# Performance work log

Measured on AMD Instinct MI355X. Metric: run time of the kernel, lower is better.

Reference implementation:

```python
import jax, jax.numpy as jnp
import numpy as np

BN_EPS = 1e-3  # keras BatchNormalization default epsilon


def setup_inputs() -> dict:
    key = jax.random.key(0)
    ks = jax.random.split(key, 7)
    B, W, D, H, C = 2, 32, 32, 32, 256
    x = jax.random.normal(ks[0], (B, W, D, H, C), dtype=jnp.float32)
    # Stacked params for the 4 branches: [query, key, judge, value]
    conv_w = jax.random.normal(ks[1], (4, C, C), dtype=jnp.float32) / np.sqrt(C).astype(np.float32)
    conv_b = jax.random.normal(ks[2], (4, C), dtype=jnp.float32) * 0.01
    bn_scale = 1.0 + 0.1 * jax.random.normal(ks[3], (4, C), dtype=jnp.float32)
    bn_offset = 0.1 * jax.random.normal(ks[4], (4, C), dtype=jnp.float32)
    bn_mean = 0.1 * jax.random.normal(ks[5], (4, C), dtype=jnp.float32)
    bn_var = jax.random.uniform(ks[6], (4, C), dtype=jnp.float32, minval=0.5, maxval=1.5)
    gamma = jnp.asarray(1e-4, dtype=jnp.float32)  # scalar residual scale (init 0.0001 in source)
    return dict(x=x, conv_w=conv_w, conv_b=conv_b, bn_scale=bn_scale,
                bn_offset=bn_offset, bn_mean=bn_mean, bn_var=bn_var, gamma=gamma)


def _branch(x, w, b, s, o, m, v):
    # Conv3D 1x1x1 == per-voxel channel mixing, then inference-mode BN, then ReLU
    y = jnp.einsum('bwdhc,cf->bwdhf', x, w) + b
    y = s * (y - m) * jax.lax.rsqrt(v + BN_EPS) + o
    return jax.nn.relu(y)


def reference(x, conv_w, conv_b, bn_scale, bn_offset, bn_mean, bn_var, gamma):
    B, W, D, H, C = x.shape
    N = W * D * H
    # Raw reshape (B,W,D,H,C) -> (B,C,N), matching keras Reshape((C,-1)) on channels-last layout
    def br(i):
        return _branch(x, conv_w[i], conv_b[i], bn_scale[i], bn_offset[i],
                       bn_mean[i], bn_var[i]).reshape(B, C, N)
    Q, K, J, V = br(0), br(1), br(2), br(3)
    m1 = jnp.matmul(K, jnp.swapaxes(Q, 1, 2))   # (B, C, C)
    m2 = jnp.matmul(K, jnp.swapaxes(J, 1, 2))   # (B, C, C)
    affinity = jax.nn.sigmoid(jnp.matmul(m1, m2))  # (B, C, C), sigmoid not softmax
    weights = jnp.matmul(affinity, V)           # (B, C, N)
    weights = weights.reshape(B, W, D, H, C)    # raw reshape back, as in source
    return gamma * weights + x
```

## Files before the change

### kernel.cpp

```cpp
#include <hip/hip_runtime.h>
#include <math.h>

typedef __attribute__((ext_vector_type(4))) float  f32x4;
typedef __attribute__((ext_vector_type(8))) short  s16x8;
typedef __attribute__((ext_vector_type(4))) short  s16x4;

#define BN_EPS 1e-3f

static constexpr int    CC    = 256;
static constexpr int    NVOX  = 32768;
static constexpr int    BATCH = 2;
static constexpr int    MTOT  = BATCH * NVOX;
static constexpr size_t ELEM_BR = (size_t)MTOT * CC;
static constexpr size_t SZ_BR   = ELEM_BR * 2;
static constexpr size_t WS_Q   = 0;
static constexpr size_t WS_K   = WS_Q  + SZ_BR;
static constexpr size_t WS_J   = WS_K  + SZ_BR;
static constexpr size_t WS_V   = WS_J  + SZ_BR;
static constexpr size_t WS_M1  = WS_V  + SZ_BR;
static constexpr size_t WS_M2  = WS_M1 + (size_t)BATCH*CC*CC*4;
static constexpr size_t WS_AFF = WS_M2 + (size_t)BATCH*CC*CC*4;
static constexpr size_t WS_WT  = WS_AFF + (size_t)BATCH*CC*CC*2;
static constexpr size_t WS_AB  = WS_WT + (size_t)4*CC*CC*2;

__device__ __forceinline__ short f2bf(float f) {
  union { float f; unsigned u; } v; v.f = f;
  unsigned u = v.u + 0x7FFFu + ((v.u >> 16) & 1u);
  return (short)(u >> 16);
}

__global__ __launch_bounds__(256) void k0_prep(
    const float* __restrict__ conv_w, const float* __restrict__ conv_b,
    const float* __restrict__ bn_s, const float* __restrict__ bn_o,
    const float* __restrict__ bn_m, const float* __restrict__ bn_v,
    char* __restrict__ ws)
{
  int t = blockIdx.x * 256 + threadIdx.x;
  ((float*)(ws + WS_M1))[t] = 0.f;
  int f = t >> 16, rem = t & 65535;
  int cin = rem >> 8, cout = rem & 255;
  ((short*)(ws + WS_WT))[f*65536 + cout*256 + cin] = f2bf(conv_w[t]);
  if (t < 1024) {
    float alpha = bn_s[t] * rsqrtf(bn_v[t] + BN_EPS);
    float beta  = alpha * (conv_b[t] - bn_m[t]) + bn_o[t];
    float* ab = (float*)(ws + WS_AB);
    ab[t] = alpha; ab[1024 + t] = beta;
  }
}

__global__ __launch_bounds__(256, 2) void k1_branches(
    const float* __restrict__ x, char* __restrict__ ws)
{
  __shared__ short As[64 * 256];
  __shared__ short Bs[64 * 256];
  __shared__ short Rs[64][72];

  const int tid = threadIdx.x;
  const int m0  = blockIdx.x * 64;
  const int lane = tid & 63, wid = tid >> 6;
  const int wm = wid >> 1, wn = wid & 1;
  const int lr = lane & 15, lg = lane >> 4;

  const short* Wt = (const short*)(ws + WS_WT);
  const float* ab = (const float*)(ws + WS_AB);

  #pragma unroll
  for (int it = 0; it < 16; ++it) {
    int idx = tid + 256 * it;
    int r = idx >> 6, c4 = (idx & 63) << 2;
    const float4 v = *(const float4*)(x + (size_t)(m0 + r) * 256 + c4);
    s16x4 s; s[0]=f2bf(v.x); s[1]=f2bf(v.y); s[2]=f2bf(v.z); s[3]=f2bf(v.w);
    int u = c4 >> 3;
    int swz = ((u ^ ((r & 7) << 2)) << 3) | (c4 & 7);
    *(s16x4*)&As[r * 256 + swz] = s;
  }

  {
    const short* Wf = Wt;
    #pragma unroll
    for (int i = 0; i < 8; ++i) {
      int slot = i * 256 + tid;
      int cout = slot >> 5, u = slot & 31;
      int usrc = u ^ ((cout & 7) << 2);
      const short* src = Wf + cout * 256 + usrc * 8;
      short* dst = Bs + (size_t)(i * 256 + wid * 64) * 8;
      __builtin_amdgcn_global_load_lds(
          (const __attribute__((address_space(1))) void*)src,
          (__attribute__((address_space(3))) void*)dst, 16, 0, 0);
    }
  }

  __syncthreads();

  for (int nt = 0; nt < 16; ++nt) {
    const int f  = nt >> 2;
    const int c0 = (nt & 3) * 64;

    f32x4 acc[2][2];
    #pragma unroll
    for (int a = 0; a < 2; ++a)
      #pragma unroll
      for (int b = 0; b < 2; ++b) { f32x4 z = {0.f,0.f,0.f,0.f}; acc[a][b] = z; }

    #pragma unroll
    for (int k0 = 0; k0 < 8; ++k0) {
      const int ua = k0 * 4 + lg;
      s16x8 af[2], bf[2];
      #pragma unroll
      for (int mi = 0; mi < 2; ++mi) {
        int r = wm*32 + mi*16 + lr;
        int uu = ua ^ ((r & 7) << 2);
        af[mi] = *(const s16x8*)&As[r * 256 + uu * 8];
      }
      #pragma unroll
      for (int nj = 0; nj < 2; ++nj) {
        int c = wn*32 + nj*16 + lr;
        int uu = ua ^ ((c & 7) << 2);
        bf[nj] = *(const s16x8*)&Bs[c * 256 + uu * 8];
      }
      #pragma unroll
      for (int mi = 0; mi < 2; ++mi)
        #pragma unroll
        for (int nj = 0; nj < 2; ++nj)
          acc[mi][nj] = __builtin_amdgcn_mfma_f32_16x16x32_bf16(
              bf[nj], af[mi], acc[mi][nj], 0, 0, 0);
    }

    __syncthreads();

    if (nt < 15) {
      const int fn  = (nt + 1) >> 2;
      const int c0n = ((nt + 1) & 3) * 64;
      const short* Wf = Wt + fn * 65536 + c0n * 256;
      #pragma unroll
      for (int i = 0; i < 8; ++i) {
        int slot = i * 256 + tid;
        int cout = slot >> 5, u = slot & 31;
        int usrc = u ^ ((cout & 7) << 2);
        const short* src = Wf + cout * 256 + usrc * 8;
        short* dst = Bs + (size_t)(i * 256 + wid * 64) * 8;
        __builtin_amdgcn_global_load_lds(
            (const __attribute__((address_space(1))) void*)src,
            (__attribute__((address_space(3))) void*)dst, 16, 0, 0);
      }
    }

    #pragma unroll
    for (int nj = 0; nj < 2; ++nj) {
      int c4b = c0 + wn*32 + nj*16 + lg*4;
      const f32x4 al = *(const f32x4*)&ab[f*256 + c4b];
      const f32x4 be = *(const f32x4*)&ab[1024 + f*256 + c4b];
      #pragma unroll
      for (int mi = 0; mi < 2; ++mi) {
        s16x4 s;
        #pragma unroll
        for (int ii = 0; ii < 4; ++ii) {
          float yv = al[ii] * acc[mi][nj][ii] + be[ii];
          yv = yv > 0.f ? yv : 0.f;
          s[ii] = f2bf(yv);
        }
        *(s16x4*)&Rs[wm*32 + mi*16 + lr][wn*32 + nj*16 + lg*4] = s;
      }
    }

    __syncthreads();

    short* Yf = (short*)(ws + (size_t)f * SZ_BR);
    #pragma unroll
    for (int it = 0; it < 2; ++it) {
      int idx = tid + 256 * it;
      int r = idx >> 3, c8 = (idx & 7) << 3;
      *(s16x8*)&Yf[(size_t)(m0 + r) * 256 + c0 + c8] = *(const s16x8*)&Rs[r][c8];
    }
  }
}

__global__ __launch_bounds__(256, 2) void k2_m1m2(char* __restrict__ ws)
{
  __shared__ short Ks[128 * 64];
  __shared__ short Qs[128 * 64];
  __shared__ short Js[128 * 64];

  const int tid = threadIdx.x;
  const int chunk = blockIdx.x;
  const int ti = blockIdx.y >> 1, tj = blockIdx.y & 1;
  const int b  = blockIdx.z;
  const size_t boff = (size_t)b * NVOX * CC;
  const short* Km = (const short*)(ws + WS_K) + boff + (size_t)(ti*128) * NVOX;
  const short* Qm = (const short*)(ws + WS_Q) + boff + (size_t)(tj*128) * NVOX;
  const short* Jm = (const short*)(ws + WS_J) + boff + (size_t)(tj*128) * NVOX;

  const int lane = tid & 63, wid = tid >> 6;
  const int wm = wid >> 1, wn = wid & 1;
  const int lr = lane & 15, lg = lane >> 4;

  f32x4 accq[4][4], accj[4][4];
  #pragma unroll
  for (int a = 0; a < 4; ++a)
    #pragma unroll
    for (int c = 0; c < 4; ++c) { f32x4 z = {0.f,0.f,0.f,0.f}; accq[a][c] = z; accj[a][c] = z; }

  for (int t = 0; t < 8; ++t) {
    const int n0 = chunk * 512 + t * 64;
    __syncthreads();
    #pragma unroll
    for (int i = 0; i < 4; ++i) {
      int slot = i * 256 + tid;
      int r = slot >> 3, u = slot & 7;
      int usrc = u ^ (r & 7);
      const size_t so = (size_t)r * NVOX + n0 + usrc * 8;
      short* dK = Ks + (size_t)(i * 256 + wid * 64) * 8;
      short* dQ = Qs + (size_t)(i * 256 + wid * 64) * 8;
      short* dJ = Js + (size_t)(i * 256 + wid * 64) * 8;
      __builtin_amdgcn_global_load_lds(
          (const __attribute__((address_space(1))) void*)(Km + so),
          (__attribute__((address_space(3))) void*)dK, 16, 0, 0);
      __builtin_amdgcn_global_load_lds(
          (const __attribute__((address_space(1))) void*)(Qm + so),
          (__attribute__((address_space(3))) void*)dQ, 16, 0, 0);
      __builtin_amdgcn_global_load_lds(
          (const __attribute__((address_space(1))) void*)(Jm + so),
          (__attribute__((address_space(3))) void*)dJ, 16, 0, 0);
    }
    __syncthreads();
    #pragma unroll
    for (int ks = 0; ks < 2; ++ks) {
      const int ua = ks * 4 + lg;
      s16x8 a[4], bq[4], bj[4];
      #pragma unroll
      for (int mi = 0; mi < 4; ++mi) {
        int r = wm*64 + mi*16 + lr;
        a[mi] = *(const s16x8*)&Ks[r * 64 + (ua ^ (r & 7)) * 8];
      }
      #pragma unroll
      for (int nj = 0; nj < 4; ++nj) {
        int r = wn*64 + nj*16 + lr;
        bq[nj] = *(const s16x8*)&Qs[r * 64 + (ua ^ (r & 7)) * 8];
        bj[nj] = *(const s16x8*)&Js[r * 64 + (ua ^ (r & 7)) * 8];
      }
      #pragma unroll
      for (int mi = 0; mi < 4; ++mi)
        #pragma unroll
        for (int nj = 0; nj < 4; ++nj) {
          accq[mi][nj] = __builtin_amdgcn_mfma_f32_16x16x32_bf16(a[mi], bq[nj], accq[mi][nj], 0,0,0);
          accj[mi][nj] = __builtin_amdgcn_mfma_f32_16x16x32_bf16(a[mi], bj[nj], accj[mi][nj], 0,0,0);
        }
    }
  }
  float* m1 = (float*)(ws + WS_M1) + (size_t)b * CC * CC;
  float* m2 = (float*)(ws + WS_M2) + (size_t)b * CC * CC;
  #pragma unroll
  for (int mi = 0; mi < 4; ++mi)
    #pragma unroll
    for (int nj = 0; nj < 4; ++nj)
      #pragma unroll
      for (int ii = 0; ii < 4; ++ii) {
        int i = ti*128 + wm*64 + mi*16 + lg*4 + ii;
        int j = tj*128 + wn*64 + nj*16 + lr;
        atomicAdd(&m1[i*256 + j], accq[mi][nj][ii]);
        atomicAdd(&m2[i*256 + j], accj[mi][nj][ii]);
      }
}

__global__ __launch_bounds__(256) void k3_aff(char* __restrict__ ws)
{
  const int j = threadIdx.x;
  const int i = blockIdx.x & 255;
  const int b = blockIdx.x >> 8;
  const float* m1 = (const float*)(ws + WS_M1) + (size_t)b * CC * CC;
  const float* m2 = (const float*)(ws + WS_M2) + (size_t)b * CC * CC;
  float z = 0.f;
  #pragma unroll 8
  for (int k = 0; k < 256; ++k)
    z = fmaf(m1[i*256 + k], m2[k*256 + j], z);
  float a = 1.f / (1.f + expf(-z));
  ((short*)(ws + WS_AFF))[(size_t)b*CC*CC + i*256 + j] = f2bf(a);
}

__global__ __launch_bounds__(512, 4) void k4_out(
    const float* __restrict__ x, const float* __restrict__ gamma_p,
    char* __restrict__ ws, float* __restrict__ out)
{
  __shared__ short affS[256][72];
  __shared__ short Vs[128][72];

  const int tid = threadIdx.x;
  const int n0 = blockIdx.x * 128;
  const int b  = blockIdx.y;
  const float gamma = gamma_p[0];
  const short* aff = (const short*)(ws + WS_AFF) + (size_t)b * CC * CC;
  const short* Vm  = (const short*)(ws + WS_V) + (size_t)b * NVOX * CC;

  const int lane = tid & 63, wid = tid >> 6;
  const int wi = wid >> 1, wn = wid & 1;
  const int lr = lane & 15, lg = lane >> 4;

  f32x4 acc[4][4];
  #pragma unroll
  for (int a = 0; a < 4; ++a)
    #pragma unroll
    for (int c = 0; c < 4; ++c) { f32x4 z = {0.f,0.f,0.f,0.f}; acc[a][c] = z; }

  for (int c0 = 0; c0 < 256; c0 += 64) {
    __syncthreads();
    #pragma unroll
    for (int it = 0; it < 4; ++it) {
      int idx = tid + 512 * it;
      int r = idx >> 3, c8 = (idx & 7) << 3;
      *(s16x8*)&affS[r][c8] = *(const s16x8*)&aff[(size_t)r * 256 + c0 + c8];
    }
    #pragma unroll
    for (int it = 0; it < 2; ++it) {
      int idx = tid + 512 * it;
      int t15 = idx & 15;
      int cc = idx >> 4, n8 = t15 << 3;
      s16x8 v = *(const s16x8*)&Vm[(size_t)(c0 + cc) * NVOX + n0 + n8];
      #pragma unroll
      for (int uu = 0; uu < 8; ++uu) {
        int u = (uu + t15) & 7;
        Vs[n8 + u][cc] = v[u];
      }
    }
    __syncthreads();
    #pragma unroll
    for (int ks = 0; ks < 2; ++ks) {
      s16x8 af[4], bv[4];
      #pragma unroll
      for (int mi = 0; mi < 4; ++mi)
        af[mi] = *(const s16x8*)&affS[wi*64 + mi*16 + lr][ks*32 + lg*8];
      #pragma unroll
      for (int nj = 0; nj < 4; ++nj)
        bv[nj] = *(const s16x8*)&Vs[wn*64 + nj*16 + lr][ks*32 + lg*8];
      #pragma unroll
      for (int mi = 0; mi < 4; ++mi)
        #pragma unroll
        for (int nj = 0; nj < 4; ++nj)
          acc[mi][nj] = __builtin_amdgcn_mfma_f32_16x16x32_bf16(
              bv[nj], af[mi], acc[mi][nj], 0, 0, 0);
    }
  }
  #pragma unroll
  for (int mi = 0; mi < 4; ++mi)
    #pragma unroll
    for (int nj = 0; nj < 4; ++nj) {
      int i = wi*64 + mi*16 + lr;
      int n = n0 + wn*64 + nj*16 + lg*4;
      size_t flat = (size_t)b * NVOX * CC + (size_t)i * NVOX + n;
      const float4 xv = *(const float4*)(x + flat);
      float4 o;
      o.x = gamma * acc[mi][nj][0] + xv.x;
      o.y = gamma * acc[mi][nj][1] + xv.y;
      o.z = gamma * acc[mi][nj][2] + xv.z;
      o.w = gamma * acc[mi][nj][3] + xv.w;
      *(float4*)(out + flat) = o;
    }
}

extern "C" void kernel_launch(void* const* d_in, const int* in_sizes, int n_in,
                              void* d_out, int out_size, void* d_ws, size_t ws_size,
                              hipStream_t stream)
{
  const float* x      = (const float*)d_in[0];
  const float* conv_w = (const float*)d_in[1];
  const float* conv_b = (const float*)d_in[2];
  const float* bn_s   = (const float*)d_in[3];
  const float* bn_o   = (const float*)d_in[4];
  const float* bn_m   = (const float*)d_in[5];
  const float* bn_v   = (const float*)d_in[6];
  const float* gamma  = (const float*)d_in[7];
  char*  ws  = (char*)d_ws;
  float* out = (float*)d_out;

  k0_prep    <<<1024, 256, 0, stream>>>(conv_w, conv_b, bn_s, bn_o, bn_m, bn_v, ws);
  k1_branches<<<1024, 256, 0, stream>>>(x, ws);
  k2_m1m2    <<<dim3(64, 4, 2), 256, 0, stream>>>(ws);
  k3_aff     <<<512, 256, 0, stream>>>(ws);
  k4_out     <<<dim3(256, 2), 512, 0, stream>>>(x, gamma, ws, out);
}
```

Baseline: 198.0 us.

## Restructure K·Qᵀ/K·Jᵀ kernel with double buffering and partial-sum reduction

The m1/m2 kernel now uses 512-thread blocks that each compute the full 256x256 product for one matrix (Q or J) over one N-chunk. Shared-memory tiles are double-buffered so global-to-LDS loads of the next tile overlap the MFMA work on the current one. When the workspace is large enough, the fp32 atomicAdds are replaced by bf16 partial outputs per chunk, summed in a separate reduction kernel. This removes atomic contention but adds a 64-way partial write/read pass, bf16 rounding of the partials, and an extra launch.

Measured after the change: 166.6 us, median of 2. -15.9%, faster.

```diff
diff --git a/kernel.cpp b/kernel.cpp
--- a/kernel.cpp
+++ b/kernel.cpp
@@ -22,11 +22,17 @@
 static constexpr size_t WS_AFF = WS_M2 + (size_t)BATCH*CC*CC*4;
 static constexpr size_t WS_WT  = WS_AFF + (size_t)BATCH*CC*CC*2;
 static constexpr size_t WS_AB  = WS_WT + (size_t)4*CC*CC*2;
+static constexpr size_t WS_P   = WS_AB + 2048*4;
+static constexpr size_t WS_NEED_PART = WS_P + (size_t)4*64*65536*2;
 
 __device__ __forceinline__ short f2bf(float f) {
   union { float f; unsigned u; } v; v.f = f;
   unsigned u = v.u + 0x7FFFu + ((v.u >> 16) & 1u);
   return (short)(u >> 16);
+}
+__device__ __forceinline__ float bf2f(short s) {
+  union { unsigned u; float f; } v; v.u = ((unsigned)(unsigned short)s) << 16;
+  return v.f;
 }
 
 __global__ __launch_bounds__(256) void k0_prep(
@@ -175,91 +181,134 @@
   }
 }
 
-__global__ __launch_bounds__(256, 2) void k2_m1m2(char* __restrict__ ws)
-{
-  __shared__ short Ks[128 * 64];
-  __shared__ short Qs[128 * 64];
-  __shared__ short Js[128 * 64];
+template<int PART>
+__global__ __launch_bounds__(512, 2) void k2_m1m2(char* __restrict__ ws)
+{
+  __shared__ short Ks[2][16384];
+  __shared__ short Xs[2][16384];
 
   const int tid = threadIdx.x;
   const int chunk = blockIdx.x;
-  const int ti = blockIdx.y >> 1, tj = blockIdx.y & 1;
-  const int b  = blockIdx.z;
+  const int mat = blockIdx.y;
+  const int b   = blockIdx.z;
   const size_t boff = (size_t)b * NVOX * CC;
-  const short* Km = (const short*)(ws + WS_K) + boff + (size_t)(ti*128) * NVOX;
-  const short* Qm = (const short*)(ws + WS_Q) + boff + (size_t)(tj*128) * NVOX;
-  const short* Jm = (const short*)(ws + WS_J) + boff + (size_t)(tj*128) * NVOX;
+  const short* Km = (const short*)(ws + WS_K) + boff;
+  const short* Xm = (const short*)(ws + (mat ? WS_J : WS_Q)) + boff;
 
   const int lane = tid & 63, wid = tid >> 6;
   const int wm = wid >> 1, wn = wid & 1;
   const int lr = lane & 15, lg = lane >> 4;
 
-  f32x4 accq[4][4], accj[4][4];
+  f32x4 acc[4][8];
   #pragma unroll
   for (int a = 0; a < 4; ++a)
     #pragma unroll
-    for (int c = 0; c < 4; ++c) { f32x4 z = {0.f,0.f,0.f,0.f}; accq[a][c] = z; accj[a][c] = z; }
-
-  for (int t = 0; t < 8; ++t) {
-    const int n0 = chunk * 512 + t * 64;
-    __syncthreads();
+    for (int c = 0; c < 8; ++c) { f32x4 z = {0.f,0.f,0.f,0.f}; acc[a][c] = z; }
+
+  {
+    const int n0 = chunk * 512;
     #pragma unroll
     for (int i = 0; i < 4; ++i) {
-      int slot = i * 256 + tid;
+      int slot = i * 512 + tid;
       int r = slot >> 3, u = slot & 7;
       int usrc = u ^ (r & 7);
       const size_t so = (size_t)r * NVOX + n0 + usrc * 8;
-      short* dK = Ks + (size_t)(i * 256 + wid * 64) * 8;
-      short* dQ = Qs + (size_t)(i * 256 + wid * 64) * 8;
-      short* dJ = Js + (size_t)(i * 256 + wid * 64) * 8;
+      short* dK = Ks[0] + (size_t)(i * 512 + wid * 64) * 8;
+      short* dX = Xs[0] + (size_t)(i * 512 + wid * 64) * 8;
       __builtin_amdgcn_global_load_lds(
           (const __attribute__((address_space(1))) void*)(Km + so),
           (__attribute__((address_space(3))) void*)dK, 16, 0, 0);
       __builtin_amdgcn_global_load_lds(
-          (const __attribute__((address_space(1))) void*)(Qm + so),
-          (__attribute__((address_space(3))) void*)dQ, 16, 0, 0);
-      __builtin_amdgcn_global_load_lds(
-          (const __attribute__((address_space(1))) void*)(Jm + so),
-          (__attribute__((address_space(3))) void*)dJ, 16, 0, 0);
-    }
-    __syncthreads();
+          (const __attribute__((address_space(1))) void*)(Xm + so),
+          (__attribute__((address_space(3))) void*)dX, 16, 0, 0);
+    }
+  }
+  __syncthreads();
+
+  for (int t = 0; t < 8; ++t) {
+    const int cur = t & 1;
+    if (t < 7) {
+      const int n0n = chunk * 512 + (t + 1) * 64;
+      const int nxt = cur ^ 1;
+      #pragma unroll
+      for (int i = 0; i < 4; ++i) {
+        int slot = i * 512 + tid;
+        int r = slot >> 3, u = slot & 7;
+        int usrc = u ^ (r & 7);
+        const size_t so = (size_t)r * NVOX + n0n + usrc * 8;
+        short* dK = Ks[nxt] + (size_t)(i * 512 + wid * 64) * 8;
+        short* dX = Xs[nxt] + (size_t)(i * 512 + wid * 64) * 8;
+        __builtin_amdgcn_global_load_lds(
+            (const __attribute__((address_space(1))) void*)(Km + so),
+            (__attribute__((address_space(3))) void*)dK, 16, 0, 0);
+        __builtin_amdgcn_global_load_lds(
+            (const __attribute__((address_space(1))) void*)(Xm + so),
+            (__attribute__((address_space(3))) void*)dX, 16, 0, 0);
+      }
+    }
     #pragma unroll
     for (int ks = 0; ks < 2; ++ks) {
       const int ua = ks * 4 + lg;
-      s16x8 a[4], bq[4], bj[4];
+      s16x8 a[4], xf[8];
       #pragma unroll
       for (int mi = 0; mi < 4; ++mi) {
         int r = wm*64 + mi*16 + lr;
-        a[mi] = *(const s16x8*)&Ks[r * 64 + (ua ^ (r & 7)) * 8];
-      }
-      #pragma unroll
-      for (int nj = 0; nj < 4; ++nj) {
-        int r = wn*64 + nj*16 + lr;
-        bq[nj] = *(const s16x8*)&Qs[r * 64 + (ua ^ (r & 7)) * 8];
-        bj[nj] = *(const s16x8*)&Js[r * 64 + (ua ^ (r & 7)) * 8];
+        a[mi] = *(const s16x8*)&Ks[cur][r * 64 + (ua ^ (r & 7)) * 8];
+      }
+      #pragma unroll
+      for (int nj = 0; nj < 8; ++nj) {
+        int r = wn*128 + nj*16 + lr;
+        xf[nj] = *(const s16x8*)&Xs[cur][r * 64 + (ua ^ (r & 7)) * 8];
       }
       #pragma unroll
       for (int mi = 0; mi < 4; ++mi)
         #pragma unroll
-        for (int nj = 0; nj < 4; ++nj) {
-          accq[mi][nj] = __builtin_amdgcn_mfma_f32_16x16x32_bf16(a[mi], bq[nj], accq[mi][nj], 0,0,0);
-          accj[mi][nj] = __builtin_amdgcn_mfma_f32_16x16x32_bf16(a[mi], bj[nj], accj[mi][nj], 0,0,0);
-        }
-    }
-  }
-  float* m1 = (float*)(ws + WS_M1) + (size_t)b * CC * CC;
-  float* m2 = (float*)(ws + WS_M2) + (size_t)b * CC * CC;
-  #pragma unroll
-  for (int mi = 0; mi < 4; ++mi)
-    #pragma unroll
-    for (int nj = 0; nj < 4; ++nj)
-      #pragma unroll
-      for (int ii = 0; ii < 4; ++ii) {
-        int i = ti*128 + wm*64 + mi*16 + lg*4 + ii;
-        int j = tj*128 + wn*64 + nj*16 + lr;
-        atomicAdd(&m1[i*256 + j], accq[mi][nj][ii]);
-        atomicAdd(&m2[i*256 + j], accj[mi][nj][ii]);
-      }
+        for (int nj = 0; nj < 8; ++nj)
+          acc[mi][nj] = __builtin_amdgcn_mfma_f32_16x16x32_bf16(
+              a[mi], xf[nj], acc[mi][nj], 0, 0, 0);
+    }
+    __syncthreads();
+  }
+
+  if (PART) {
+    short* P = (short*)(ws + WS_P) + ((size_t)((mat*2 + b)*64 + chunk)) * 65536;
+    #pragma unroll
+    for (int mi = 0; mi < 4; ++mi)
+      #pragma unroll
+      for (int nj = 0; nj < 8; ++nj) {
+        int i = wm*64 + mi*16 + lg*4;
+        int j = wn*128 + nj*16 + lr;
+        #pragma unroll
+        for (int ii = 0; ii < 4; ++ii)
+          P[(size_t)(i + ii) * 256 + j] = f2bf(acc[mi][nj][ii]);
+      }
+  } else {
+    float* M = (float*)(ws + (mat ? WS_M2 : WS_M1)) + (size_t)b * CC * CC;
+    #pragma unroll
+    for (int mi = 0; mi < 4; ++mi)
+      #pragma unroll
+      for (int nj = 0; nj < 8; ++nj) {
+        int i = wm*64 + mi*16 + lg*4;
+        int j = wn*128 + nj*16 + lr;
+        #pragma unroll
+        for (int ii = 0; ii < 4; ++ii)
+          atomicAdd(&M[(size_t)(i + ii) * 256 + j], acc[mi][nj][ii]);
+      }
+  }
+}
+
+__global__ __launch_bounds__(256) void k25_reduce(char* __restrict__ ws)
+{
+  int idx = blockIdx.x * 256 + threadIdx.x;
+  int mb = idx >> 16;
+  int ij = idx & 65535;
+  const short* P = (const short*)(ws + WS_P) + ((size_t)mb * 64) * 65536 + ij;
+  float s = 0.f;
+  #pragma unroll 8
+  for (int c = 0; c < 64; ++c)
+    s += bf2f(P[(size_t)c * 65536]);
+  float* dst = (float*)(ws + ((mb >> 1) ? WS_M2 : WS_M1)) + (size_t)(mb & 1) * 65536 + ij;
+  *dst = s;
 }
 
 __global__ __launch_bounds__(256) void k3_aff(char* __restrict__ ws)
@@ -371,9 +420,16 @@
   char*  ws  = (char*)d_ws;
   float* out = (float*)d_out;
 
+  const bool part = ws_size >= WS_NEED_PART;
+
   k0_prep    <<<1024, 256, 0, stream>>>(conv_w, conv_b, bn_s, bn_o, bn_m, bn_v, ws);
   k1_branches<<<1024, 256, 0, stream>>>(x, ws);
-  k2_m1m2    <<<dim3(64, 4, 2), 256, 0, stream>>>(ws);
+  if (part) {
+    k2_m1m2<1><<<dim3(64, 2, 2), 512, 0, stream>>>(ws);
+    k25_reduce<<<1024, 256, 0, stream>>>(ws);
+  } else {
+    k2_m1m2<0><<<dim3(64, 2, 2), 512, 0, stream>>>(ws);
+  }
   k3_aff     <<<512, 256, 0, stream>>>(ws);
   k4_out     <<<dim3(256, 2), 512, 0, stream>>>(x, gamma, ws, out);
 }
```
